# Optimization experiments

Hardware: AMD Instinct MI355X
Metric: run time of the kernel (lower is better)

Reference implementation:

```python
import jax, jax.numpy as jnp
import numpy as np

B, S, E, HD = 32, 1024, 768, 64
NUM_IMAGE_PATCHES = 49


def setup_inputs() -> dict:
    key = jax.random.key(0)
    ks = jax.random.split(key, 9)
    w = 0.02
    return {
        "decoder_sequence": jax.random.normal(ks[0], (B, S, E), dtype=jnp.float32),
        "Wq": jax.random.normal(ks[1], (E, HD), dtype=jnp.float32) * w,
        "bq": jnp.zeros((HD,), dtype=jnp.float32),
        "Wk": jax.random.normal(ks[2], (E, HD), dtype=jnp.float32) * w,
        "bk": jnp.zeros((HD,), dtype=jnp.float32),
        "Wv": jax.random.normal(ks[3], (E, HD), dtype=jnp.float32) * w,
        "bv": jnp.zeros((HD,), dtype=jnp.float32),
        "input_sequence_length": 975,
        "padding_mask": jax.random.randint(ks[4], (B, 1, S), 0, 2).astype(bool),
    }


def reference(decoder_sequence, Wq, bq, Wk, bk, Wv, bv, input_sequence_length, padding_mask):
    # single-head projections: [B,S,E] @ [E,HD] -> [B,S,HD]
    Q = decoder_sequence @ Wq + bq
    K = decoder_sequence @ Wk + bk
    V = decoder_sequence @ Wv + bv

    scores = jnp.einsum('bid,bjd->bij', Q, K) / jnp.sqrt(jnp.float32(HD))

    # mask: image-patch rows (i < 49) fully unmasked; text region is causal
    # (mask[49:,49:] = triu(-inf, diag=1)), i.e. -inf where i >= 49 and j > i.
    i = jnp.arange(S)[:, None]
    j = jnp.arange(S)[None, :]
    causal_bad = (i >= NUM_IMAGE_PATCHES) & (j > i)  # [S,S]
    scores = jnp.where(causal_bad[None, :, :], -jnp.inf, scores)

    # padding mask on keys, broadcast over queries: [B,1,S] -> [B,S,S]
    scores = jnp.where(padding_mask, -jnp.inf, scores)

    A = jax.nn.softmax(scores, axis=-1)
    H = jnp.einsum('bij,bjd->bid', A, V)
    return H
```

## Files before the change

### kernel.cpp

```cpp
#include <hip/hip_runtime.h>
#include <stdint.h>
#include <stddef.h>


typedef __attribute__((ext_vector_type(8))) short bf16x8;
typedef __attribute__((ext_vector_type(4))) float f32x4;

#define NIP 49
#define QSCALE 0.18033688011112042f

#define GLDS16(g, l)                                      \
  __builtin_amdgcn_global_load_lds(                       \
      (const __attribute__((address_space(1))) void*)(g), \
      (__attribute__((address_space(3))) void*)(l), 16, 0, 0)

__device__ __forceinline__ short f2b(float f) {
  union { float f; uint32_t u; } c; c.f = f;
  uint32_t u = c.u;
  uint32_t r = (u + 0x7fffu + ((u >> 16) & 1u)) >> 16;
  return (short)(uint16_t)r;
}

__global__ __launch_bounds__(256) void wt_kernel(
    const float* __restrict__ Wq, const float* __restrict__ Wk,
    const float* __restrict__ Wv, short* __restrict__ Wt) {
  int idx = blockIdx.x * 256 + threadIdx.x;
  int n = idx / 768;
  int k = idx - n * 768;
  const float* W = (n < 64) ? Wq : (n < 128) ? Wk : Wv;
  Wt[idx] = f2b(W[(size_t)k * 64 + (n & 63)]);
}

__global__ __launch_bounds__(512, 4) void proj_kernel(
    const float* __restrict__ X, const float* __restrict__ bq,
    const float* __restrict__ bk, const float* __restrict__ bv,
    const short* __restrict__ Wt, short* __restrict__ Qg,
    short* __restrict__ Kg, short* __restrict__ Vt) {
  __shared__ short lX[2][2][64][32];
  __shared__ short lW[2][2][192][32];
  const int tid = threadIdx.x;
  const int wid = tid >> 6, lane = tid & 63;
  const int l15 = lane & 15, q4 = lane >> 4;
  const int mw = wid & 3;
  const int nh = wid >> 2;
  const int r0 = blockIdx.x * 64;

  const int xi0 = tid, xi1 = tid + 512;
  float4 rx0, rx1;
  auto xload = [&](int kb) {
    rx0 = *(const float4*)(X + (size_t)(r0 + (xi0 >> 4)) * 768 + kb + (xi0 & 15) * 4);
    rx1 = *(const float4*)(X + (size_t)(r0 + (xi1 >> 4)) * 768 + kb + (xi1 & 15) * 4);
  };
  auto xstage = [&](int buf) {
    short4 s0, s1;
    s0.x = f2b(rx0.x); s0.y = f2b(rx0.y); s0.z = f2b(rx0.z); s0.w = f2b(rx0.w);
    s1.x = f2b(rx1.x); s1.y = f2b(rx1.y); s1.z = f2b(rx1.z); s1.w = f2b(rx1.w);
    *(short4*)&lX[buf][(xi0 & 15) >> 3][xi0 >> 4][(xi0 & 7) * 4] = s0;
    *(short4*)&lX[buf][(xi1 & 15) >> 3][xi1 >> 4][(xi1 & 7) * 4] = s1;
  };
  const int wr = lane >> 2, wc = (lane & 3) * 8;
  auto wlds = [&](int buf, int kb) {
#pragma unroll
    for (int i = 0; i < 3; ++i) {
      const int fi = wid * 3 + i;
      const int j = fi >> 1, ks = fi & 1;
      GLDS16(Wt + (size_t)(j * 16 + wr) * 768 + kb + ks * 32 + wc,
             &lW[buf][ks][j * 16][0]);
    }
  };

  f32x4 acc[6];
#pragma unroll
  for (int c = 0; c < 6; ++c) acc[c] = (f32x4){0.f, 0.f, 0.f, 0.f};

  xload(0);
  wlds(0, 0);
  xstage(0);
  __syncthreads();

#pragma unroll
  for (int st = 0; st < 12; ++st) {
    const int cur = st & 1;
    if (st + 1 < 12) {
      xload((st + 1) * 64);
      wlds(cur ^ 1, (st + 1) * 64);
    }
#pragma unroll
    for (int ks = 0; ks < 2; ++ks) {
      bf16x8 a = *(const bf16x8*)&lX[cur][ks][mw * 16 + l15][q4 * 8];
#pragma unroll
      for (int c = 0; c < 6; ++c) {
        bf16x8 bw = *(const bf16x8*)&lW[cur][ks][(nh * 6 + c) * 16 + l15][q4 * 8];
        acc[c] = __builtin_amdgcn_mfma_f32_16x16x32_bf16(a, bw, acc[c], 0, 0, 0);
      }
    }
    if (st + 1 < 12) xstage(cur ^ 1);
    __syncthreads();
  }

  const int b = r0 >> 10, s0 = r0 & 1023;
#pragma unroll
  for (int c = 0; c < 6; ++c) {
    const int ct = nh * 6 + c;
    const int mtx = ct >> 2;
    const int h = (ct & 3) * 16 + l15;
    if (mtx < 2) {
      const float bias = (mtx == 0 ? bq : bk)[h];
      short* op = (mtx == 0) ? Qg : Kg;
#pragma unroll
      for (int rr = 0; rr < 4; ++rr) {
        int row = r0 + mw * 16 + q4 * 4 + rr;
        float v = acc[c][rr] + bias;
        if (mtx == 0) v *= QSCALE;
        op[(size_t)row * 64 + h] = f2b(v);
      }
    } else {
      const float bias = bv[h];
      short4 sv;
      sv.x = f2b(acc[c][0] + bias); sv.y = f2b(acc[c][1] + bias);
      sv.z = f2b(acc[c][2] + bias); sv.w = f2b(acc[c][3] + bias);
      *(short4*)(Vt + ((size_t)(b * 64 + h) << 10) + s0 + mw * 16 + q4 * 4) = sv;
    }
  }
}

__global__ __launch_bounds__(256, 3) void attn_kernel(
    const short* __restrict__ Qg, const short* __restrict__ Kg,
    const short* __restrict__ Vt, const int* __restrict__ pad,
    float* __restrict__ out) {
  __shared__ short lK[2][2][64][32];
  __shared__ short lV[2][2][80][32];
  __shared__ short lP[4][16][68];

  const int b = blockIdx.x;
  const int level = blockIdx.y;
  const int t = (level == 0) ? 0 : 16 - level;
  const int tid = threadIdx.x;
  const int wid = tid >> 6, lane = tid & 63;
  const int l15 = lane & 15, q4 = lane >> 4;
  const int qs = t * 64;
  const size_t base = (size_t)b * 1024;
  const int nkt = (t == 0) ? 16 : (t + 1);

#pragma unroll
  for (int i = 0; i < 8; ++i) {
    int idx = tid + i * 256;
    int buf = idx >> 10, rem = idx & 1023;
    int h = rem >> 9, r = (rem >> 5) & 15, cc = rem & 31;
    lV[buf][h][64 + r][cc] = (r == 0) ? (short)0x3F80 : (short)0;
  }

  const short* qrow = Qg + (base + qs + wid * 16 + l15) * 64;
  bf16x8 aq0 = *(const bf16x8*)(qrow + q4 * 8);
  bf16x8 aq1 = *(const bf16x8*)(qrow + 32 + q4 * 8);

  const int sr = lane >> 2, sc = (lane & 3) * 8;
  auto wlds_tile = [&](int buf, int kt) {
    const int kb = kt * 64;
#pragma unroll
    for (int h = 0; h < 2; ++h) {
      GLDS16(Kg + (base + kb + wid * 16 + sr) * 64 + h * 32 + sc,
             &lK[buf][h][wid * 16][0]);
      GLDS16(Vt + ((size_t)(b * 64 + wid * 16 + sr) << 10) + kb + h * 32 + sc,
             &lV[buf][h][wid * 16][0]);
    }
  };
  int pc[4];
  auto pload = [&](int kt) {
#pragma unroll
    for (int c = 0; c < 4; ++c) pc[c] = pad[base + kt * 64 + c * 16 + l15];
  };

  pload(0);
  wlds_tile(0, 0);
  __syncthreads();

  f32x4 o[5];
#pragma unroll
  for (int c = 0; c < 5; ++c) o[c] = (f32x4){0.f, 0.f, 0.f, 0.f};

  for (int kt = 0; kt < nkt; ++kt) {
    const int cur = kt & 1;
    const int kb = kt * 64;
    float padm[4];
#pragma unroll
    for (int c = 0; c < 4; ++c) padm[c] = (pc[c] != 0) ? 0.f : 1.f;
    if (kt + 1 < nkt) {
      wlds_tile(cur ^ 1, kt + 1);
      pload(kt + 1);
    }

    f32x4 s4[4];
#pragma unroll
    for (int c = 0; c < 4; ++c) {
      s4[c] = (f32x4){0.f, 0.f, 0.f, 0.f};
      bf16x8 b0 = *(const bf16x8*)&lK[cur][0][c * 16 + l15][q4 * 8];
      s4[c] = __builtin_amdgcn_mfma_f32_16x16x32_bf16(aq0, b0, s4[c], 0, 0, 0);
      bf16x8 b1 = *(const bf16x8*)&lK[cur][1][c * 16 + l15][q4 * 8];
      s4[c] = __builtin_amdgcn_mfma_f32_16x16x32_bf16(aq1, b1, s4[c], 0, 0, 0);
    }

    const bool diag = (kt == t);
    const bool img = (t == 0 && kt > 0);
#pragma unroll
    for (int rr = 0; rr < 4; ++rr) {
      const int qi = qs + wid * 16 + q4 * 4 + rr;
#pragma unroll
      for (int c = 0; c < 4; ++c) {
        float p = exp2f(fminf(s4[c][rr], 80.f)) * padm[c];
        if (diag) {
          int j = kb + c * 16 + l15;
          if (qi >= NIP && j > qi) p = 0.f;
        }
        if (img && qi >= NIP) p = 0.f;
        lP[wid][q4 * 4 + rr][c * 16 + l15] = f2b(p);
      }
    }

    bf16x8 ap0 = *(const bf16x8*)&lP[wid][l15][q4 * 8];
    bf16x8 ap1 = *(const bf16x8*)&lP[wid][l15][32 + q4 * 8];
#pragma unroll
    for (int c = 0; c < 5; ++c) {
      bf16x8 b0 = *(const bf16x8*)&lV[cur][0][c * 16 + l15][q4 * 8];
      o[c] = __builtin_amdgcn_mfma_f32_16x16x32_bf16(ap0, b0, o[c], 0, 0, 0);
      bf16x8 b1 = *(const bf16x8*)&lV[cur][1][c * 16 + l15][q4 * 8];
      o[c] = __builtin_amdgcn_mfma_f32_16x16x32_bf16(ap1, b1, o[c], 0, 0, 0);
    }
    __syncthreads();
  }

#pragma unroll
  for (int rr = 0; rr < 4; ++rr) {
    float l = __shfl(o[4][rr], lane & 48, 64);
    const float inv = (l > 0.f) ? 1.0f / l : 0.f;
    const size_t row = base + qs + wid * 16 + q4 * 4 + rr;
#pragma unroll
    for (int c = 0; c < 4; ++c)
      out[row * 64 + c * 16 + l15] = o[c][rr] * inv;
  }
}

extern "C" void kernel_launch(void* const* d_in, const int* in_sizes, int n_in,
                              void* d_out, int out_size, void* d_ws, size_t ws_size,
                              hipStream_t stream) {
  const float* X  = (const float*)d_in[0];
  const float* Wq = (const float*)d_in[1];
  const float* bq = (const float*)d_in[2];
  const float* Wk = (const float*)d_in[3];
  const float* bk = (const float*)d_in[4];
  const float* Wv = (const float*)d_in[5];
  const float* bv = (const float*)d_in[6];
  const int* pad  = (const int*)d_in[8];
  float* out = (float*)d_out;

  short* Qg = (short*)d_ws;
  short* Kg = Qg + 32768 * 64;
  short* Vt = Kg + 32768 * 64;
  short* Wt = Vt + 32768 * 64;

  wt_kernel<<<576, 256, 0, stream>>>(Wq, Wk, Wv, Wt);
  proj_kernel<<<512, 512, 0, stream>>>(X, bq, bk, bv, Wt, Qg, Kg, Vt);
  attn_kernel<<<dim3(32, 16), 256, 0, stream>>>(Qg, Kg, Vt, pad, out);
}
```

Before: 202.5 us.

## Widen attention key tiles to 128 and give each projection wave all columns

The attention kernel now loads 128-key tiles per step instead of 64. This halves the number of loop iterations and barrier syncs, and processes the softmax-times-V product in two 64-key halves. The row-sum column of ones moves from padded V rows into a separate small shared buffer. The projection kernel drops to 256 threads per block, with each wave computing all 12 output column tiles for its 16 rows, which reuses the X fragment across more MFMAs. In exchange, register pressure rises, occupancy targets drop, and odd query tiles now compute some fully masked keys.

Result: no change. 201.7 us (-0.4%).

```diff
diff --git a/kernel.cpp b/kernel.cpp
--- a/kernel.cpp
+++ b/kernel.cpp
@@ -31,7 +31,7 @@
   Wt[idx] = f2b(W[(size_t)k * 64 + (n & 63)]);
 }
 
-__global__ __launch_bounds__(512, 4) void proj_kernel(
+__global__ __launch_bounds__(256, 2) void proj_kernel(
     const float* __restrict__ X, const float* __restrict__ bq,
     const float* __restrict__ bk, const float* __restrict__ bv,
     const short* __restrict__ Wt, short* __restrict__ Qg,
@@ -41,37 +41,39 @@
   const int tid = threadIdx.x;
   const int wid = tid >> 6, lane = tid & 63;
   const int l15 = lane & 15, q4 = lane >> 4;
-  const int mw = wid & 3;
-  const int nh = wid >> 2;
   const int r0 = blockIdx.x * 64;
 
-  const int xi0 = tid, xi1 = tid + 512;
-  float4 rx0, rx1;
+  float4 rx[4];
   auto xload = [&](int kb) {
-    rx0 = *(const float4*)(X + (size_t)(r0 + (xi0 >> 4)) * 768 + kb + (xi0 & 15) * 4);
-    rx1 = *(const float4*)(X + (size_t)(r0 + (xi1 >> 4)) * 768 + kb + (xi1 & 15) * 4);
+#pragma unroll
+    for (int i = 0; i < 4; ++i) {
+      const int xi = tid + i * 256;
+      rx[i] = *(const float4*)(X + (size_t)(r0 + (xi >> 4)) * 768 + kb + (xi & 15) * 4);
+    }
   };
   auto xstage = [&](int buf) {
-    short4 s0, s1;
-    s0.x = f2b(rx0.x); s0.y = f2b(rx0.y); s0.z = f2b(rx0.z); s0.w = f2b(rx0.w);
-    s1.x = f2b(rx1.x); s1.y = f2b(rx1.y); s1.z = f2b(rx1.z); s1.w = f2b(rx1.w);
-    *(short4*)&lX[buf][(xi0 & 15) >> 3][xi0 >> 4][(xi0 & 7) * 4] = s0;
-    *(short4*)&lX[buf][(xi1 & 15) >> 3][xi1 >> 4][(xi1 & 7) * 4] = s1;
+#pragma unroll
+    for (int i = 0; i < 4; ++i) {
+      const int xi = tid + i * 256;
+      short4 s;
+      s.x = f2b(rx[i].x); s.y = f2b(rx[i].y); s.z = f2b(rx[i].z); s.w = f2b(rx[i].w);
+      *(short4*)&lX[buf][(xi & 15) >> 3][xi >> 4][(xi & 7) * 4] = s;
+    }
   };
   const int wr = lane >> 2, wc = (lane & 3) * 8;
   auto wlds = [&](int buf, int kb) {
 #pragma unroll
-    for (int i = 0; i < 3; ++i) {
-      const int fi = wid * 3 + i;
+    for (int i = 0; i < 6; ++i) {
+      const int fi = wid * 6 + i;
       const int j = fi >> 1, ks = fi & 1;
       GLDS16(Wt + (size_t)(j * 16 + wr) * 768 + kb + ks * 32 + wc,
              &lW[buf][ks][j * 16][0]);
     }
   };
 
-  f32x4 acc[6];
-#pragma unroll
-  for (int c = 0; c < 6; ++c) acc[c] = (f32x4){0.f, 0.f, 0.f, 0.f};
+  f32x4 acc[12];
+#pragma unroll
+  for (int c = 0; c < 12; ++c) acc[c] = (f32x4){0.f, 0.f, 0.f, 0.f};
 
   xload(0);
   wlds(0, 0);
@@ -87,10 +89,10 @@
     }
 #pragma unroll
     for (int ks = 0; ks < 2; ++ks) {
-      bf16x8 a = *(const bf16x8*)&lX[cur][ks][mw * 16 + l15][q4 * 8];
-#pragma unroll
-      for (int c = 0; c < 6; ++c) {
-        bf16x8 bw = *(const bf16x8*)&lW[cur][ks][(nh * 6 + c) * 16 + l15][q4 * 8];
+      bf16x8 a = *(const bf16x8*)&lX[cur][ks][wid * 16 + l15][q4 * 8];
+#pragma unroll
+      for (int c = 0; c < 12; ++c) {
+        bf16x8 bw = *(const bf16x8*)&lW[cur][ks][c * 16 + l15][q4 * 8];
         acc[c] = __builtin_amdgcn_mfma_f32_16x16x32_bf16(a, bw, acc[c], 0, 0, 0);
       }
     }
@@ -100,16 +102,15 @@
 
   const int b = r0 >> 10, s0 = r0 & 1023;
 #pragma unroll
-  for (int c = 0; c < 6; ++c) {
-    const int ct = nh * 6 + c;
-    const int mtx = ct >> 2;
-    const int h = (ct & 3) * 16 + l15;
+  for (int c = 0; c < 12; ++c) {
+    const int mtx = c >> 2;
+    const int h = (c & 3) * 16 + l15;
     if (mtx < 2) {
       const float bias = (mtx == 0 ? bq : bk)[h];
       short* op = (mtx == 0) ? Qg : Kg;
 #pragma unroll
       for (int rr = 0; rr < 4; ++rr) {
-        int row = r0 + mw * 16 + q4 * 4 + rr;
+        int row = r0 + wid * 16 + q4 * 4 + rr;
         float v = acc[c][rr] + bias;
         if (mtx == 0) v *= QSCALE;
         op[(size_t)row * 64 + h] = f2b(v);
@@ -119,18 +120,19 @@
       short4 sv;
       sv.x = f2b(acc[c][0] + bias); sv.y = f2b(acc[c][1] + bias);
       sv.z = f2b(acc[c][2] + bias); sv.w = f2b(acc[c][3] + bias);
-      *(short4*)(Vt + ((size_t)(b * 64 + h) << 10) + s0 + mw * 16 + q4 * 4) = sv;
-    }
-  }
-}
-
-__global__ __launch_bounds__(256, 3) void attn_kernel(
+      *(short4*)(Vt + ((size_t)(b * 64 + h) << 10) + s0 + wid * 16 + q4 * 4) = sv;
+    }
+  }
+}
+
+__global__ __launch_bounds__(256, 2) void attn_kernel(
     const short* __restrict__ Qg, const short* __restrict__ Kg,
     const short* __restrict__ Vt, const int* __restrict__ pad,
     float* __restrict__ out) {
-  __shared__ short lK[2][2][64][32];
-  __shared__ short lV[2][2][80][32];
+  __shared__ short lK[2][2][128][32];
+  __shared__ short lV[2][4][64][32];
   __shared__ short lP[4][16][68];
+  __shared__ short lOnes[16][32];
 
   const int b = blockIdx.x;
   const int level = blockIdx.y;
@@ -140,14 +142,12 @@
   const int l15 = lane & 15, q4 = lane >> 4;
   const int qs = t * 64;
   const size_t base = (size_t)b * 1024;
-  const int nkt = (t == 0) ? 16 : (t + 1);
-
-#pragma unroll
-  for (int i = 0; i < 8; ++i) {
-    int idx = tid + i * 256;
-    int buf = idx >> 10, rem = idx & 1023;
-    int h = rem >> 9, r = (rem >> 5) & 15, cc = rem & 31;
-    lV[buf][h][64 + r][cc] = (r == 0) ? (short)0x3F80 : (short)0;
+  const int nkt = (t == 0) ? 8 : (t / 2 + 1);
+
+  {
+    int i0 = tid, i1 = tid + 256;
+    ((short*)lOnes)[i0] = ((i0 >> 5) == 0) ? (short)0x3F80 : (short)0;
+    if (i1 < 512) ((short*)lOnes)[i1] = ((i1 >> 5) == 0) ? (short)0x3F80 : (short)0;
   }
 
   const short* qrow = Qg + (base + qs + wid * 16 + l15) * 64;
@@ -156,19 +156,23 @@
 
   const int sr = lane >> 2, sc = (lane & 3) * 8;
   auto wlds_tile = [&](int buf, int kt) {
-    const int kb = kt * 64;
-#pragma unroll
-    for (int h = 0; h < 2; ++h) {
-      GLDS16(Kg + (base + kb + wid * 16 + sr) * 64 + h * 32 + sc,
-             &lK[buf][h][wid * 16][0]);
-      GLDS16(Vt + ((size_t)(b * 64 + wid * 16 + sr) << 10) + kb + h * 32 + sc,
-             &lV[buf][h][wid * 16][0]);
-    }
-  };
-  int pc[4];
+    const int kb = kt * 128;
+#pragma unroll
+    for (int i = 0; i < 4; ++i) {
+      const int dh = i & 1, krow = wid * 32 + (i >> 1) * 16;
+      GLDS16(Kg + (base + kb + krow + sr) * 64 + dh * 32 + sc,
+             &lK[buf][dh][krow][0]);
+    }
+#pragma unroll
+    for (int kq = 0; kq < 4; ++kq) {
+      GLDS16(Vt + ((size_t)(b * 64 + wid * 16 + sr) << 10) + kb + kq * 32 + sc,
+             &lV[buf][kq][wid * 16][0]);
+    }
+  };
+  int pc[8];
   auto pload = [&](int kt) {
 #pragma unroll
-    for (int c = 0; c < 4; ++c) pc[c] = pad[base + kt * 64 + c * 16 + l15];
+    for (int c = 0; c < 8; ++c) pc[c] = pad[base + kt * 128 + c * 16 + l15];
   };
 
   pload(0);
@@ -181,18 +185,18 @@
 
   for (int kt = 0; kt < nkt; ++kt) {
     const int cur = kt & 1;
-    const int kb = kt * 64;
-    float padm[4];
-#pragma unroll
-    for (int c = 0; c < 4; ++c) padm[c] = (pc[c] != 0) ? 0.f : 1.f;
+    const int kb = kt * 128;
+    float padm[8];
+#pragma unroll
+    for (int c = 0; c < 8; ++c) padm[c] = (pc[c] != 0) ? 0.f : 1.f;
     if (kt + 1 < nkt) {
       wlds_tile(cur ^ 1, kt + 1);
       pload(kt + 1);
     }
 
-    f32x4 s4[4];
-#pragma unroll
-    for (int c = 0; c < 4; ++c) {
+    f32x4 s4[8];
+#pragma unroll
+    for (int c = 0; c < 8; ++c) {
       s4[c] = (f32x4){0.f, 0.f, 0.f, 0.f};
       bf16x8 b0 = *(const bf16x8*)&lK[cur][0][c * 16 + l15][q4 * 8];
       s4[c] = __builtin_amdgcn_mfma_f32_16x16x32_bf16(aq0, b0, s4[c], 0, 0, 0);
@@ -200,31 +204,43 @@
       s4[c] = __builtin_amdgcn_mfma_f32_16x16x32_bf16(aq1, b1, s4[c], 0, 0, 0);
     }
 
-    const bool diag = (kt == t);
+    const bool diag = (t == 0) ? (kt == 0) : (kt == nkt - 1);
     const bool img = (t == 0 && kt > 0);
+    float p[8][4];
 #pragma unroll
     for (int rr = 0; rr < 4; ++rr) {
       const int qi = qs + wid * 16 + q4 * 4 + rr;
 #pragma unroll
-      for (int c = 0; c < 4; ++c) {
-        float p = exp2f(fminf(s4[c][rr], 80.f)) * padm[c];
+      for (int c = 0; c < 8; ++c) {
+        float pv = exp2f(fminf(s4[c][rr], 80.f)) * padm[c];
         if (diag) {
           int j = kb + c * 16 + l15;
-          if (qi >= NIP && j > qi) p = 0.f;
+          if (qi >= NIP && j > qi) pv = 0.f;
         }
-        if (img && qi >= NIP) p = 0.f;
-        lP[wid][q4 * 4 + rr][c * 16 + l15] = f2b(p);
-      }
-    }
-
-    bf16x8 ap0 = *(const bf16x8*)&lP[wid][l15][q4 * 8];
-    bf16x8 ap1 = *(const bf16x8*)&lP[wid][l15][32 + q4 * 8];
-#pragma unroll
-    for (int c = 0; c < 5; ++c) {
-      bf16x8 b0 = *(const bf16x8*)&lV[cur][0][c * 16 + l15][q4 * 8];
-      o[c] = __builtin_amdgcn_mfma_f32_16x16x32_bf16(ap0, b0, o[c], 0, 0, 0);
-      bf16x8 b1 = *(const bf16x8*)&lV[cur][1][c * 16 + l15][q4 * 8];
-      o[c] = __builtin_amdgcn_mfma_f32_16x16x32_bf16(ap1, b1, o[c], 0, 0, 0);
+        if (img && qi >= NIP) pv = 0.f;
+        p[c][rr] = pv;
+      }
+    }
+
+#pragma unroll
+    for (int half = 0; half < 2; ++half) {
+#pragma unroll
+      for (int rr = 0; rr < 4; ++rr)
+#pragma unroll
+        for (int c = 0; c < 4; ++c)
+          lP[wid][q4 * 4 + rr][c * 16 + l15] = f2b(p[half * 4 + c][rr]);
+      bf16x8 ap0 = *(const bf16x8*)&lP[wid][l15][q4 * 8];
+      bf16x8 ap1 = *(const bf16x8*)&lP[wid][l15][32 + q4 * 8];
+      const int kq0 = half * 2, kq1 = half * 2 + 1;
+#pragma unroll
+      for (int c = 0; c < 5; ++c) {
+        bf16x8 b0 = (c < 4) ? *(const bf16x8*)&lV[cur][kq0][c * 16 + l15][q4 * 8]
+                            : *(const bf16x8*)&lOnes[l15][q4 * 8];
+        o[c] = __builtin_amdgcn_mfma_f32_16x16x32_bf16(ap0, b0, o[c], 0, 0, 0);
+        bf16x8 b1 = (c < 4) ? *(const bf16x8*)&lV[cur][kq1][c * 16 + l15][q4 * 8]
+                            : *(const bf16x8*)&lOnes[l15][q4 * 8];
+        o[c] = __builtin_amdgcn_mfma_f32_16x16x32_bf16(ap1, b1, o[c], 0, 0, 0);
+      }
     }
     __syncthreads();
   }
@@ -259,6 +275,6 @@
   short* Wt = Vt + 32768 * 64;
 
   wt_kernel<<<576, 256, 0, stream>>>(Wq, Wk, Wv, Wt);
-  proj_kernel<<<512, 512, 0, stream>>>(X, bq, bk, bv, Wt, Qg, Kg, Vt);
+  proj_kernel<<<512, 256, 0, stream>>>(X, bq, bk, bv, Wt, Qg, Kg, Vt);
   attn_kernel<<<dim3(32, 16), 256, 0, stream>>>(Qg, Kg, Vt, pad, out);
 }
```
